# Optimization experiments

Hardware: AMD Instinct MI355X
Metric: run time of the kernel (lower is better)

The kernel has to match this reference:

```python
import jax, jax.numpy as jnp
import numpy as np

EPS = 1e-8  # F.cosine_similarity default eps


def setup_inputs() -> dict:
    key = jax.random.key(0)
    k1, k2, k3, k4 = jax.random.split(key, 4)
    Q, P, E, V = 4096, 16384, 128, 30000
    query = jax.random.randint(k1, (Q,), 0, V, dtype=jnp.int64)
    para = jax.random.randint(k2, (P,), 0, V, dtype=jnp.int64)
    que_embed = jax.random.normal(k3, (Q, E), dtype=jnp.float32)
    para_embed = jax.random.normal(k4, (P, E), dtype=jnp.float32)
    return {"query": query, "para": para, "que_embed": que_embed, "para_embed": para_embed}


def reference(query, para, que_embed, para_embed):
    # xor_matrix[i, j] = 1 if query[i] == para[j] else 0  -> [Q, P] int64
    xor_matrix = (query[:, None] == para[None, :]).astype(jnp.int64)
    # cos_matrix[i, j] = cosine_similarity(que_embed[i], para_embed[j])
    # torch semantics: dot / (max(||q||, eps) * max(||p||, eps))
    q_norm = jnp.maximum(jnp.linalg.norm(que_embed, axis=-1), EPS)   # [Q]
    p_norm = jnp.maximum(jnp.linalg.norm(para_embed, axis=-1), EPS)  # [P]
    dots = jnp.einsum('qe,pe->qp', que_embed, para_embed)            # [Q, P]
    cos_matrix = dots / (q_norm[:, None] * p_norm[None, :])
    return xor_matrix, cos_matrix
```

## Files before the change

kernel.cpp:

```cpp
#include <hip/hip_runtime.h>
#include <stdint.h>

typedef __attribute__((ext_vector_type(8))) short bf16x8;
typedef __attribute__((ext_vector_type(4))) float f32x4;

__device__ __forceinline__ uint32_t f2bf(float f) {
    uint32_t u = __builtin_bit_cast(uint32_t, f);
    u += 0x7fffu + ((u >> 16) & 1u);
    return u >> 16;
}
__device__ __forceinline__ uint32_t pack2(float a, float b) {
    return f2bf(a) | (f2bf(b) << 16);
}

__global__ __launch_bounds__(256) void prep_norms(const float* __restrict__ qe,
                                                  const float* __restrict__ pe,
                                                  float* __restrict__ rq,
                                                  float* __restrict__ rp,
                                                  int Q, int Pn) {
    int gw = (blockIdx.x * 256 + threadIdx.x) >> 6;
    int lane = threadIdx.x & 63;
    if (gw >= Q + Pn) return;
    const float* src = (gw < Q) ? (qe + (size_t)gw * 128) : (pe + (size_t)(gw - Q) * 128);
    float2 v = *(const float2*)(src + lane * 2);
    float s = v.x * v.x + v.y * v.y;
#pragma unroll
    for (int off = 32; off > 0; off >>= 1) s += __shfl_down(s, off, 64);
    if (lane == 0) {
        float r = 1.0f / fmaxf(sqrtf(s), 1e-8f);
        if (gw < Q) rq[gw] = r; else rp[gw - Q] = r;
    }
}

__global__ __launch_bounds__(256) void conv_frag(const float* __restrict__ src,
                                                 unsigned short* __restrict__ dst,
                                                 int ngroups) {
    int t = blockIdx.x * 256 + threadIdx.x;
    if (t >= ngroups * 256) return;
    int g = t >> 8, rem = t & 255;
    int c = rem >> 6, lane = rem & 63;
    int row = g * 16 + (lane & 15);
    int col = c * 32 + ((lane >> 4) << 3);
    const float* s = src + (size_t)row * 128 + col;
    float4 a0 = *(const float4*)s;
    float4 a1 = *(const float4*)(s + 4);
    uint4 pk = { pack2(a0.x, a0.y), pack2(a0.z, a0.w),
                 pack2(a1.x, a1.y), pack2(a1.z, a1.w) };
    *(uint4*)(dst + (size_t)t * 8) = pk;
}

#define PBLK 2048

__global__ __launch_bounds__(256, 4) void fused_gemm(
        const unsigned short* __restrict__ Qf, const unsigned short* __restrict__ Pf,
        const int* __restrict__ qid, const int* __restrict__ pid,
        const float* __restrict__ rq, const float* __restrict__ rp,
        float* __restrict__ oxor, float* __restrict__ ocos, int Pn) {
    __shared__ __align__(16) float scos[4 * 16 * 65];

    const int nwg = gridDim.x;
    const int chunk = nwg >> 3;
    const int bid = blockIdx.x;
    const int wg = (bid & 7) * chunk + (bid >> 3);
    const int nPc = Pn / PBLK;
    const int qg = wg / nPc;
    const int pc = wg % nPc;
    const int pblock = pc * PBLK;

    const int t = threadIdx.x;
    const int lane = t & 63;
    const int w = t >> 6;
    const int lq = lane & 15;
    const int g4 = (lane >> 4) << 2;
    const int wbase = w * (16 * 65);

    bf16x8 af[4];
    const unsigned short* abase = Qf + ((size_t)(qg * 4) * 64 + lane) * 8;
#pragma unroll
    for (int kk = 0; kk < 4; ++kk)
        af[kk] = *(const bf16x8*)(abase + kk * 512);

    const int qrow_base = qg * 16;
    const float rqv = rq[qrow_base + lq];

    for (int fl = 0; fl < PBLK / 256; ++fl) {
        const int pw = pblock + fl * 256 + w * 64;
#pragma unroll
        for (int f = 0; f < 4; ++f) {
            const int p0 = pw + f * 16;
            const unsigned short* bbase = Pf + (size_t)(p0 >> 4) * 2048 + (size_t)lane * 8;
            bf16x8 bfr[4];
#pragma unroll
            for (int kk = 0; kk < 4; ++kk)
                bfr[kk] = *(const bf16x8*)(bbase + kk * 512);
            f32x4 acc = {0.f, 0.f, 0.f, 0.f};
#pragma unroll
            for (int kk = 0; kk < 4; ++kk)
                acc = __builtin_amdgcn_mfma_f32_16x16x32_bf16(bfr[kk], af[kk], acc, 0, 0, 0);
            const float4 rpv = *(const float4*)(rp + p0 + g4);
            const int a0 = wbase + lq * 65 + f * 16 + g4;
            scos[a0 + 0] = acc[0] * rqv * rpv.x;
            scos[a0 + 1] = acc[1] * rqv * rpv.y;
            scos[a0 + 2] = acc[2] * rqv * rpv.z;
            scos[a0 + 3] = acc[3] * rqv * rpv.w;
        }
        const int pvl = pid[pw + lane];
#pragma unroll
        for (int r = 0; r < 16; ++r) {
            const int qvr = qid[qrow_base + r];
            const size_t obase = (size_t)(qrow_base + r) * Pn + pw;
            float vc = scos[wbase + r * 65 + lane];
            float vx = (qvr == pvl) ? 1.f : 0.f;
            __builtin_nontemporal_store(vc, ocos + obase + lane);
            __builtin_nontemporal_store(vx, oxor + obase + lane);
        }
    }
}

extern "C" void kernel_launch(void* const* d_in, const int* in_sizes, int n_in,
                              void* d_out, int out_size, void* d_ws, size_t ws_size,
                              hipStream_t stream) {
    const int*   qid = (const int*)d_in[0];
    const int*   pid = (const int*)d_in[1];
    const float* qe  = (const float*)d_in[2];
    const float* pe  = (const float*)d_in[3];
    const int Q  = in_sizes[0];
    const int Pn = in_sizes[1];

    unsigned short* Qf = (unsigned short*)d_ws;
    unsigned short* Pf = Qf + (size_t)Q * 128;
    float* rq = (float*)(Pf + (size_t)Pn * 128);
    float* rp = rq + Q;

    float* oxor = (float*)d_out;
    float* ocos = oxor + (size_t)Q * (size_t)Pn;

    const int qgroups = Q / 16, pgroups = Pn / 16;
    conv_frag<<<qgroups, 256, 0, stream>>>(qe, Qf, qgroups);
    conv_frag<<<pgroups, 256, 0, stream>>>(pe, Pf, pgroups);
    prep_norms<<<(Q + Pn + 3) / 4, 256, 0, stream>>>(qe, pe, rq, rp, Q, Pn);

    const int nblocks = (Q / 16) * (Pn / PBLK);
    fused_gemm<<<nblocks, 256, 0, stream>>>(Qf, Pf, qid, pid, rq, rp, oxor, ocos, Pn);
}
```

Before: 132.3 us.

## Split xor output into memset plus sparse scatter, widen cos GEMM tiles

Removes the xor matrix from the fused GEMM kernel. The xor output is now zeroed with hipMemsetAsync, and a separate kernel scatters ones only where query and para ids match. The cos GEMM uses larger P blocks (8192), 16-byte vectorized LDS and global stores, and a different occupancy bound. The memset still writes the full 256MB xor buffer, but it can do so at memset bandwidth. The qg = wg & 255 mapping hardcodes Q/16 = 256, and the plain stores drop the nontemporal hint.

```diff
diff --git a/kernel.cpp b/kernel.cpp
--- a/kernel.cpp
+++ b/kernel.cpp
@@ -49,22 +49,43 @@
     *(uint4*)(dst + (size_t)t * 8) = pk;
 }
 
-#define PBLK 2048
+__global__ __launch_bounds__(256) void xor_scatter(const int* __restrict__ qid,
+                                                   const int* __restrict__ pid,
+                                                   float* __restrict__ oxor,
+                                                   int Q, int Pn) {
+    int T = blockIdx.x * 256 + threadIdx.x;
+    int q = T >> 6;
+    if (q >= Q) return;
+    const int qv = qid[q];
+    const int stripe = Pn >> 6;
+    const int p0 = (T & 63) * stripe;
+    const size_t base = (size_t)q * Pn;
+    const int4* pp = (const int4*)(pid + p0);
+#pragma unroll 4
+    for (int i = 0; i < 64; ++i) {
+        int4 pv = pp[i];
+        int p = p0 + i * 4;
+        if (pv.x == qv) oxor[base + p]     = 1.f;
+        if (pv.y == qv) oxor[base + p + 1] = 1.f;
+        if (pv.z == qv) oxor[base + p + 2] = 1.f;
+        if (pv.w == qv) oxor[base + p + 3] = 1.f;
+    }
+}
 
-__global__ __launch_bounds__(256, 4) void fused_gemm(
+#define PBLK 8192
+
+__global__ __launch_bounds__(256, 2) void cos_gemm(
         const unsigned short* __restrict__ Qf, const unsigned short* __restrict__ Pf,
-        const int* __restrict__ qid, const int* __restrict__ pid,
         const float* __restrict__ rq, const float* __restrict__ rp,
-        float* __restrict__ oxor, float* __restrict__ ocos, int Pn) {
-    __shared__ __align__(16) float scos[4 * 16 * 65];
+        float* __restrict__ ocos, int Pn) {
+    __shared__ __align__(16) float scos[4][16][260];
 
     const int nwg = gridDim.x;
     const int chunk = nwg >> 3;
     const int bid = blockIdx.x;
     const int wg = (bid & 7) * chunk + (bid >> 3);
-    const int nPc = Pn / PBLK;
-    const int qg = wg / nPc;
-    const int pc = wg % nPc;
+    const int qg = wg & 255;
+    const int pc = wg >> 8;
     const int pblock = pc * PBLK;
 
     const int t = threadIdx.x;
@@ -72,10 +93,9 @@
     const int w = t >> 6;
     const int lq = lane & 15;
     const int g4 = (lane >> 4) << 2;
-    const int wbase = w * (16 * 65);
 
     bf16x8 af[4];
-    const unsigned short* abase = Qf + ((size_t)(qg * 4) * 64 + lane) * 8;
+    const unsigned short* abase = Qf + (size_t)qg * 2048 + lane * 8;
 #pragma unroll
     for (int kk = 0; kk < 4; ++kk)
         af[kk] = *(const bf16x8*)(abase + kk * 512);
@@ -83,10 +103,10 @@
     const int qrow_base = qg * 16;
     const float rqv = rq[qrow_base + lq];
 
-    for (int fl = 0; fl < PBLK / 256; ++fl) {
-        const int pw = pblock + fl * 256 + w * 64;
-#pragma unroll
-        for (int f = 0; f < 4; ++f) {
+    for (int fl = 0; fl < PBLK / 1024; ++fl) {
+        const int pw = pblock + fl * 1024 + w * 256;
+#pragma unroll 4
+        for (int f = 0; f < 16; ++f) {
             const int p0 = pw + f * 16;
             const unsigned short* bbase = Pf + (size_t)(p0 >> 4) * 2048 + (size_t)lane * 8;
             bf16x8 bfr[4];
@@ -98,21 +118,14 @@
             for (int kk = 0; kk < 4; ++kk)
                 acc = __builtin_amdgcn_mfma_f32_16x16x32_bf16(bfr[kk], af[kk], acc, 0, 0, 0);
             const float4 rpv = *(const float4*)(rp + p0 + g4);
-            const int a0 = wbase + lq * 65 + f * 16 + g4;
-            scos[a0 + 0] = acc[0] * rqv * rpv.x;
-            scos[a0 + 1] = acc[1] * rqv * rpv.y;
-            scos[a0 + 2] = acc[2] * rqv * rpv.z;
-            scos[a0 + 3] = acc[3] * rqv * rpv.w;
+            f32x4 c4 = { acc[0]*rqv*rpv.x, acc[1]*rqv*rpv.y,
+                         acc[2]*rqv*rpv.z, acc[3]*rqv*rpv.w };
+            *(f32x4*)&scos[w][lq][f * 16 + g4] = c4;
         }
-        const int pvl = pid[pw + lane];
 #pragma unroll
         for (int r = 0; r < 16; ++r) {
-            const int qvr = qid[qrow_base + r];
-            const size_t obase = (size_t)(qrow_base + r) * Pn + pw;
-            float vc = scos[wbase + r * 65 + lane];
-            float vx = (qvr == pvl) ? 1.f : 0.f;
-            __builtin_nontemporal_store(vc, ocos + obase + lane);
-            __builtin_nontemporal_store(vx, oxor + obase + lane);
+            f32x4 vc = *(const f32x4*)&scos[w][r][lane * 4];
+            *(f32x4*)(ocos + (size_t)(qrow_base + r) * Pn + pw + lane * 4) = vc;
         }
     }
 }
@@ -135,11 +148,15 @@
     float* oxor = (float*)d_out;
     float* ocos = oxor + (size_t)Q * (size_t)Pn;
 
+    hipMemsetAsync(oxor, 0, (size_t)Q * (size_t)Pn * sizeof(float), stream);
+
     const int qgroups = Q / 16, pgroups = Pn / 16;
     conv_frag<<<qgroups, 256, 0, stream>>>(qe, Qf, qgroups);
     conv_frag<<<pgroups, 256, 0, stream>>>(pe, Pf, pgroups);
     prep_norms<<<(Q + Pn + 3) / 4, 256, 0, stream>>>(qe, pe, rq, rp, Q, Pn);
 
+    xor_scatter<<<(Q * 64) / 256, 256, 0, stream>>>(qid, pid, oxor, Q, Pn);
+
     const int nblocks = (Q / 16) * (Pn / PBLK);
-    fused_gemm<<<nblocks, 256, 0, stream>>>(Qf, Pf, qid, pid, rq, rp, oxor, ocos, Pn);
+    cos_gemm<<<nblocks, 256, 0, stream>>>(Qf, Pf, rq, rp, ocos, Pn);
 }
```

New measurement: 160.1 us. +21.1%, slower.
